# Performance work log

Hardware: AMD Instinct MI355X
Metric: run time of the kernel (lower is better)

Reference implementation:

```python
import jax, jax.numpy as jnp
import numpy as np
from jax import lax

B, C, H, W = 64, 1, 256, 256
N = H * W
K = 16384  # positive_trials
LOG_CLAMP = -100.0  # torch BCELoss clamps log terms at -100


def setup_inputs() -> dict:
    key = jax.random.key(0)
    k1, k2, k3 = jax.random.split(key, 3)
    decision_scores = jax.random.normal(k1, (B, N, 2), dtype=jnp.float32)
    s_map = jax.random.uniform(k2, (B, C, H, W), dtype=jnp.float32)
    # gumbel noise g = -log(-log(U)), matching F.gumbel_softmax sampling
    u = jax.random.uniform(k3, (B, N, 2), dtype=jnp.float32, minval=1e-10, maxval=1.0)
    gumbel_noise = -jnp.log(-jnp.log(u))
    return {"decision_scores": decision_scores, "s_map": s_map, "gumbel_noise": gumbel_noise}


def reference(decision_scores, s_map, gumbel_noise):
    # Tokenizer: b c h w -> b (h w) c
    tokens = jnp.transpose(s_map.reshape(B, C, H * W), (0, 2, 1))  # [B, N, 1]
    # soft gumbel-softmax (tau=1, hard=False), keep prob of class 0
    soft = jax.nn.softmax(decision_scores + gumbel_noise, axis=-1)[:, :, 0:1]  # [B, N, 1]
    # top-K salient token indices per sample (descending sort -> top_k)
    _, idx = lax.top_k(tokens[:, :, 0], K)  # [B, K]
    trials = jnp.zeros((B, N), dtype=tokens.dtype)
    trials = trials.at[jnp.arange(B)[:, None], idx].set(1.0)[:, :, None]  # [B, N, 1]
    # BCE with reduction='sum', log clamped at -100 like torch
    log_p = jnp.clip(jnp.log(soft), LOG_CLAMP, None)
    log_1mp = jnp.clip(jnp.log(1.0 - soft), LOG_CLAMP, None)
    loss = -jnp.sum(trials * log_p + (1.0 - trials) * log_1mp)
    return loss
```

## Files before the change

kernel.cpp:

```cpp
#include <hip/hip_runtime.h>
#include <cstdint>

#define BATCH 64
#define NPIX 65536
#define TOPK 16384
#define NB 256
#define SEGS 32
#define WLO 186
#define WHI 198
#define NWBIN (WHI - WLO + 1)
#define CAPB 192
#define NSLOT (SEGS * CAPB)
#define FCAP 1024
#define WHSTRIDE 16

__device__ __forceinline__ float block_reduce(float acc) {
    __shared__ float w[4];
    __syncthreads();
    #pragma unroll
    for (int off = 32; off > 0; off >>= 1) acc += __shfl_down(acc, off, 64);
    if ((threadIdx.x & 63) == 0) w[threadIdx.x >> 6] = acc;
    __syncthreads();
    return w[0] + w[1] + w[2] + w[3];
}

__device__ __forceinline__ float block_reduce1k(float acc) {
    __shared__ float w[16];
    __syncthreads();
    #pragma unroll
    for (int off = 32; off > 0; off >>= 1) acc += __shfl_down(acc, off, 64);
    if ((threadIdx.x & 63) == 0) w[threadIdx.x >> 6] = acc;
    __syncthreads();
    float s = 0.f;
    #pragma unroll
    for (int i = 0; i < 16; ++i) s += w[i];
    return s;
}

__device__ __forceinline__ void bce_from_d(float d, float& lp, float& llp) {
    float t = __logf(1.f + __expf(-fabsf(d)));
    lp  = fmaxf(fminf(d, 0.f) - t, -100.f);
    llp = fmaxf(-fmaxf(d, 0.f) - t, -100.f);
}

__device__ __forceinline__ int vkey(float v) {
    return (int)fminf(v * 256.0f, 255.0f);
}

__device__ __forceinline__ void stage_candidate(
    bool inwin, float v, uint32_t pix, float diff, int lane,
    uint32_t* ccount, uint32_t* bvb, uint32_t* bvi, uint32_t* bvd)
{
    unsigned long long m = __ballot(inwin);
    if (m == 0ull) return;
    uint32_t cnt = (uint32_t)__popcll(m);
    int leader = (int)__builtin_ctzll(m);
    uint32_t base = 0u;
    if (lane == leader) base = atomicAdd(ccount, cnt);
    base = (uint32_t)__shfl((int)base, leader, 64);
    if (inwin) {
        uint32_t p = base + (uint32_t)__popcll(m & ((1ull << lane) - 1ull));
        if (p < CAPB) {
            bvb[p] = __float_as_uint(v);
            bvi[p] = pix;
            bvd[p] = __float_as_uint(diff);
        }
    }
}

__global__ __launch_bounds__(256, 8) void k1_pass(
    const float4* __restrict__ sc, const float4* __restrict__ gn,
    const float2* __restrict__ tokp,
    float* __restrict__ pk1, float* __restrict__ psel, float* __restrict__ phi,
    uint32_t* __restrict__ gcc,
    uint32_t* __restrict__ cvb, uint32_t* __restrict__ cvi,
    uint32_t* __restrict__ cvd, uint32_t* __restrict__ whist,
    float* __restrict__ out)
{
    __shared__ uint32_t bvb[CAPB], bvi[CAPB], bvd[CAPB];
    __shared__ uint32_t sh_wh[NWBIN];
    __shared__ uint32_t ccount;
    const int tid  = threadIdx.x;
    const int lane = tid & 63;
    if (tid < CAPB) { bvb[tid] = 0u; bvi[tid] = 0u; bvd[tid] = 0u; }
    if (tid < NWBIN) sh_wh[tid] = 0u;
    if (tid == 0) { ccount = 0u; if (blockIdx.x == 0) out[0] = 0.f; }
    __syncthreads();

    const int b   = blockIdx.x >> 5;
    const int seg = blockIdx.x & (SEGS - 1);
    const int pairbase = b * (NPIX / 2) + seg * 1024;

    float4 S[4], G[4];
    float2 T[4];
    #pragma unroll
    for (int it = 0; it < 4; ++it) {
        int j = pairbase + it * 256 + tid;
        S[it] = sc[j];
        G[it] = gn[j];
        T[it] = tokp[j];
    }

    float acc = 0.f, asel = 0.f, chi = 0.f;
    #pragma unroll
    for (int it = 0; it < 4; ++it) {
        int px0 = (seg * 1024 + it * 256 + tid) * 2;
        {
            float d = (S[it].x + G[it].x) - (S[it].y + G[it].y);
            float lp, llp; bce_from_d(d, lp, llp);
            acc += llp;
            float diff = lp - llp;
            int k = vkey(T[it].x);
            bool hi = (k > WHI);
            asel += hi ? diff : 0.f;
            chi  += hi ? 1.f : 0.f;
            stage_candidate(!hi && (k >= WLO), T[it].x, (uint32_t)px0, diff,
                            lane, &ccount, bvb, bvi, bvd);
        }
        {
            float d = (S[it].z + G[it].z) - (S[it].w + G[it].w);
            float lp, llp; bce_from_d(d, lp, llp);
            acc += llp;
            float diff = lp - llp;
            int k = vkey(T[it].y);
            bool hi = (k > WHI);
            asel += hi ? diff : 0.f;
            chi  += hi ? 1.f : 0.f;
            stage_candidate(!hi && (k >= WLO), T[it].y, (uint32_t)(px0 + 1), diff,
                            lane, &ccount, bvb, bvi, bvd);
        }
    }
    __syncthreads();
    const uint32_t cc = ccount;
    {
        uint32_t nsl = cc < CAPB ? cc : CAPB;
        if (tid < nsl) {
            int k = vkey(__uint_as_float(bvb[tid]));
            atomicAdd(&sh_wh[k - WLO], 1u);
        }
    }
    const size_t cbase = (size_t)blockIdx.x * CAPB;
    if (tid < CAPB) {
        cvb[cbase + tid] = bvb[tid];
        cvi[cbase + tid] = bvi[tid];
        cvd[cbase + tid] = bvd[tid];
    }
    if (tid == 0) gcc[blockIdx.x] = cc;

    float t1 = block_reduce(acc);
    float t2 = block_reduce(asel);
    float t3 = block_reduce(chi);
    if (tid == 0) {
        pk1[blockIdx.x]  = t1;
        psel[blockIdx.x] = t2;
        phi[blockIdx.x]  = t3;
    }
    if (tid < NWBIN) whist[(size_t)blockIdx.x * WHSTRIDE + tid] = sh_wh[tid];
}

__global__ __launch_bounds__(1024) void k4_finalize(
    const uint32_t* __restrict__ cvb, const uint32_t* __restrict__ cvi,
    const uint32_t* __restrict__ cvd, const uint32_t* __restrict__ gcc,
    const float* __restrict__ pk1, const float* __restrict__ psel,
    const float* __restrict__ phi, const uint32_t* __restrict__ whist,
    const float4* __restrict__ tok4,
    const float2* __restrict__ sc2, const float2* __restrict__ gn2,
    float* __restrict__ out)
{
    __shared__ uint32_t fvb[FCAP], fvi[FCAP];
    __shared__ float    fdf[FCAP];
    __shared__ uint32_t fh[NB];
    __shared__ uint32_t wc[NWBIN];
    __shared__ uint32_t fcnt;
    __shared__ int      sh_sb, sh_ovf;
    __shared__ uint32_t sh_rem;

    const int b = blockIdx.x, tid = threadIdx.x;
    if (tid == 0) { fcnt = 0u; sh_sb = -1; sh_ovf = 0; sh_rem = 1u; }
    __syncthreads();

    const size_t base = (size_t)b * NSLOT;

    if (tid < SEGS && gcc[b * SEGS + tid] > CAPB) sh_ovf = 1;
    if (tid < NWBIN) {
        uint32_t u = 0;
        #pragma unroll
        for (int s = 0; s < SEGS; ++s)
            u += whist[(size_t)(b * SEGS + s) * WHSTRIDE + tid];
        wc[tid] = u;
    }
    float chl = (tid < SEGS) ? phi[b * SEGS + tid] : 0.f;
    float chf = block_reduce1k(chl);
    if (tid == 0) {
        uint32_t cnt_hi = (uint32_t)(chf + 0.5f);
        if (cnt_hi >= TOPK) sh_ovf = 1;
        else {
            uint32_t cum = cnt_hi;
            int found = -1; uint32_t rem = 1u;
            for (int jj = WHI; jj >= WLO; --jj) {
                uint32_t nc = cum + wc[jj - WLO];
                if (nc >= TOPK) { found = jj; rem = TOPK - cum; break; }
                cum = nc;
            }
            if (found < 0) sh_ovf = 1;
            else { sh_sb = found; sh_rem = rem; }
        }
    }
    __syncthreads();

    bool fast = (sh_ovf == 0);
    const int sb = sh_sb;
    float fac = (tid < SEGS) ? pk1[b * SEGS + tid] : 0.f;

    if (fast) {
        if (tid < SEGS) fac += psel[b * SEGS + tid];
        #pragma unroll
        for (int it = 0; it < NSLOT / 1024; ++it) {
            int t = it * 1024 + tid;
            uint32_t vb = cvb[base + t];
            uint32_t vd = cvd[base + t];
            int k = vkey(__uint_as_float(vb));
            if (k > sb) fac += __uint_as_float(vd);
            else if (k == sb) {
                uint32_t p = atomicAdd(&fcnt, 1u);
                if (p < FCAP) {
                    fvb[p] = vb;
                    fvi[p] = cvi[base + t] & (NPIX - 1);
                    fdf[p] = __uint_as_float(vd);
                }
            }
        }
        __syncthreads();
        if (fcnt > FCAP) fast = false;
        if (fast) {
            const uint32_t cnt = fcnt, rem = sh_rem;
            for (uint32_t j = tid; j < cnt; j += 1024) {
                const uint32_t mb = fvb[j], mi = fvi[j];
                uint32_t rank = 0;
                for (uint32_t i = 0; i < cnt; ++i) {
                    uint32_t ob = fvb[i];
                    rank += (ob > mb) || (ob == mb && fvi[i] < mi);
                }
                if (rank < rem) fac += fdf[j];
            }
        }
    }

    if (!fast) {
        fac = (tid < SEGS) ? pk1[b * SEGS + tid] : 0.f;
        for (int i = tid; i < NB; i += 1024) fh[i] = 0u;
        if (tid == 0) fcnt = 0u;
        __syncthreads();
        const float4* tbase = tok4 + (size_t)b * (NPIX / 4);
        for (int it = 0; it < NPIX / 4 / 1024; ++it) {
            float4 v = tbase[it * 1024 + tid];
            atomicAdd(&fh[vkey(v.x)], 1u);
            atomicAdd(&fh[vkey(v.y)], 1u);
            atomicAdd(&fh[vkey(v.z)], 1u);
            atomicAdd(&fh[vkey(v.w)], 1u);
        }
        __syncthreads();
        if (tid == 0) {
            uint32_t cum = 0; int bin = NB - 1;
            for (; bin > 0; --bin) {
                if (cum + fh[bin] >= TOPK) break;
                cum += fh[bin];
            }
            sh_sb = bin; sh_rem = TOPK - cum;
        }
        __syncthreads();
        const int sb2 = sh_sb; const uint32_t rem2 = sh_rem;
        for (int it = 0; it < NPIX / 4 / 1024; ++it) {
            int j = it * 1024 + tid;
            float4 v = tbase[j];
            int px = j * 4;
            float fv[4] = {v.x, v.y, v.z, v.w};
            #pragma unroll
            for (int q = 0; q < 4; ++q) {
                int k = vkey(fv[q]);
                if (k > sb2) {
                    size_t idx = (size_t)b * NPIX + (px + q);
                    float2 Sv = sc2[idx]; float2 Gv = gn2[idx];
                    float d = (Sv.x + Gv.x) - (Sv.y + Gv.y);
                    float lp, llp; bce_from_d(d, lp, llp);
                    fac += lp - llp;
                } else if (k == sb2) {
                    uint32_t p = atomicAdd(&fcnt, 1u);
                    if (p < FCAP) { fvb[p] = __float_as_uint(fv[q]); fvi[p] = (uint32_t)(px + q); }
                }
            }
        }
        __syncthreads();
        const uint32_t cnt2 = min(fcnt, (uint32_t)FCAP);
        for (uint32_t j = tid; j < cnt2; j += 1024) {
            const uint32_t mb = fvb[j], mi = fvi[j];
            uint32_t rank = 0;
            for (uint32_t i = 0; i < cnt2; ++i) {
                uint32_t ob = fvb[i];
                rank += (ob > mb) || (ob == mb && fvi[i] < mi);
            }
            if (rank < rem2) {
                size_t idx = (size_t)b * NPIX + (mi & (NPIX - 1));
                float2 Sv = sc2[idx]; float2 Gv = gn2[idx];
                float d = (Sv.x + Gv.x) - (Sv.y + Gv.y);
                float lp, llp; bce_from_d(d, lp, llp);
                fac += lp - llp;
            }
        }
    }

    float tot = block_reduce1k(fac);
    if (tid == 0) atomicAdd(out, -tot);
}

extern "C" void kernel_launch(void* const* d_in, const int* in_sizes, int n_in,
                              void* d_out, int out_size, void* d_ws, size_t ws_size,
                              hipStream_t stream) {
    const float* scores = (const float*)d_in[0];
    const float* smap   = (const float*)d_in[1];
    const float* gumbel = (const float*)d_in[2];
    float* out = (float*)d_out;

    char* ws = (char*)d_ws;
    float*    pk1   = (float*)ws;    ws += (size_t)BATCH * SEGS * 4;
    float*    psel  = (float*)ws;    ws += (size_t)BATCH * SEGS * 4;
    float*    phi   = (float*)ws;    ws += (size_t)BATCH * SEGS * 4;
    uint32_t* gcc   = (uint32_t*)ws; ws += (size_t)BATCH * SEGS * 4;
    uint32_t* cvb   = (uint32_t*)ws; ws += (size_t)BATCH * NSLOT * 4;
    uint32_t* cvi   = (uint32_t*)ws; ws += (size_t)BATCH * NSLOT * 4;
    uint32_t* cvd   = (uint32_t*)ws; ws += (size_t)BATCH * NSLOT * 4;
    uint32_t* whist = (uint32_t*)ws; ws += (size_t)BATCH * SEGS * WHSTRIDE * 4;

    k1_pass<<<BATCH * SEGS, 256, 0, stream>>>(
        (const float4*)scores, (const float4*)gumbel, (const float2*)smap,
        pk1, psel, phi, gcc, cvb, cvi, cvd, whist, out);

    k4_finalize<<<BATCH, 1024, 0, stream>>>(
        cvb, cvi, cvd, gcc, pk1, psel, phi, whist,
        (const float4*)smap, (const float2*)scores, (const float2*)gumbel, out);
}
```

Baseline: 118.7 us.

## Bucket-sort candidates by key bin in pass one and sum per-bin diffs

The first kernel now counting-sorts each block's staged candidates by window bin in shared memory and records per-bin sums of the BCE difference. The finalize kernel then adds whole bins above the split bin from those sums and reads only the candidates in the split bin, instead of scanning all 6144 slots per sample. This cuts global reads and branching in the single-block-per-sample finalize step. In exchange the first kernel gains extra barriers, shared atomics and a serial prefix scan.

New measurement: 117.3 us. About the same (-1.2%).

```diff
diff --git a/kernel.cpp b/kernel.cpp
--- a/kernel.cpp
+++ b/kernel.cpp
@@ -75,15 +75,18 @@
     uint32_t* __restrict__ gcc,
     uint32_t* __restrict__ cvb, uint32_t* __restrict__ cvi,
     uint32_t* __restrict__ cvd, uint32_t* __restrict__ whist,
+    float* __restrict__ wdsumg,
     float* __restrict__ out)
 {
     __shared__ uint32_t bvb[CAPB], bvi[CAPB], bvd[CAPB];
-    __shared__ uint32_t sh_wh[NWBIN];
+    __shared__ uint32_t qvb[CAPB], qvi[CAPB], qvd[CAPB];
+    __shared__ uint32_t sh_wh[NWBIN], sh_pref[NWBIN], sh_cur[NWBIN];
+    __shared__ float    sh_wds[NWBIN];
     __shared__ uint32_t ccount;
     const int tid  = threadIdx.x;
     const int lane = tid & 63;
-    if (tid < CAPB) { bvb[tid] = 0u; bvi[tid] = 0u; bvd[tid] = 0u; }
-    if (tid < NWBIN) sh_wh[tid] = 0u;
+    if (tid < CAPB) { qvb[tid] = 0u; qvi[tid] = 0u; qvd[tid] = 0u; }
+    if (tid < NWBIN) { sh_wh[tid] = 0u; sh_cur[tid] = 0u; sh_wds[tid] = 0.f; }
     if (tid == 0) { ccount = 0u; if (blockIdx.x == 0) out[0] = 0.f; }
     __syncthreads();
 
@@ -131,19 +134,34 @@
         }
     }
     __syncthreads();
-    const uint32_t cc = ccount;
-    {
-        uint32_t nsl = cc < CAPB ? cc : CAPB;
-        if (tid < nsl) {
-            int k = vkey(__uint_as_float(bvb[tid]));
-            atomicAdd(&sh_wh[k - WLO], 1u);
-        }
-    }
+    const uint32_t cc  = ccount;
+    const uint32_t nsl = cc < CAPB ? cc : CAPB;
+    if (tid < nsl) {
+        int k = vkey(__uint_as_float(bvb[tid]));
+        atomicAdd(&sh_wh[k - WLO], 1u);
+    }
+    __syncthreads();
+    if (tid == 0) {
+        uint32_t run = 0;
+        #pragma unroll
+        for (int i = 0; i < NWBIN; ++i) { sh_pref[i] = run; run += sh_wh[i]; }
+    }
+    __syncthreads();
+    if (tid < nsl) {
+        uint32_t vb = bvb[tid];
+        int bin = vkey(__uint_as_float(vb)) - WLO;
+        uint32_t pos = sh_pref[bin] + atomicAdd(&sh_cur[bin], 1u);
+        qvb[pos] = vb;
+        qvi[pos] = bvi[tid];
+        qvd[pos] = bvd[tid];
+        atomicAdd(&sh_wds[bin], __uint_as_float(bvd[tid]));
+    }
+    __syncthreads();
     const size_t cbase = (size_t)blockIdx.x * CAPB;
     if (tid < CAPB) {
-        cvb[cbase + tid] = bvb[tid];
-        cvi[cbase + tid] = bvi[tid];
-        cvd[cbase + tid] = bvd[tid];
+        cvb[cbase + tid] = qvb[tid];
+        cvi[cbase + tid] = qvi[tid];
+        cvd[cbase + tid] = qvd[tid];
     }
     if (tid == 0) gcc[blockIdx.x] = cc;
 
@@ -155,7 +173,10 @@
         psel[blockIdx.x] = t2;
         phi[blockIdx.x]  = t3;
     }
-    if (tid < NWBIN) whist[(size_t)blockIdx.x * WHSTRIDE + tid] = sh_wh[tid];
+    if (tid < NWBIN) {
+        whist[(size_t)blockIdx.x * WHSTRIDE + tid]  = sh_wh[tid];
+        wdsumg[(size_t)blockIdx.x * WHSTRIDE + tid] = sh_wds[tid];
+    }
 }
 
 __global__ __launch_bounds__(1024) void k4_finalize(
@@ -163,6 +184,7 @@
     const uint32_t* __restrict__ cvd, const uint32_t* __restrict__ gcc,
     const float* __restrict__ pk1, const float* __restrict__ psel,
     const float* __restrict__ phi, const uint32_t* __restrict__ whist,
+    const float* __restrict__ wdsumg,
     const float4* __restrict__ tok4,
     const float2* __restrict__ sc2, const float2* __restrict__ gn2,
     float* __restrict__ out)
@@ -171,6 +193,7 @@
     __shared__ float    fdf[FCAP];
     __shared__ uint32_t fh[NB];
     __shared__ uint32_t wc[NWBIN];
+    __shared__ uint32_t segstart[SEGS], segcnt[SEGS];
     __shared__ uint32_t fcnt;
     __shared__ int      sh_sb, sh_ovf;
     __shared__ uint32_t sh_rem;
@@ -178,8 +201,6 @@
     const int b = blockIdx.x, tid = threadIdx.x;
     if (tid == 0) { fcnt = 0u; sh_sb = -1; sh_ovf = 0; sh_rem = 1u; }
     __syncthreads();
-
-    const size_t base = (size_t)b * NSLOT;
 
     if (tid < SEGS && gcc[b * SEGS + tid] > CAPB) sh_ovf = 1;
     if (tid < NWBIN) {
@@ -209,24 +230,35 @@
     __syncthreads();
 
     bool fast = (sh_ovf == 0);
-    const int sb = sh_sb;
+    const int sb  = sh_sb;
+    const int sbi = sb - WLO;
     float fac = (tid < SEGS) ? pk1[b * SEGS + tid] : 0.f;
 
     if (fast) {
         if (tid < SEGS) fac += psel[b * SEGS + tid];
-        #pragma unroll
-        for (int it = 0; it < NSLOT / 1024; ++it) {
-            int t = it * 1024 + tid;
-            uint32_t vb = cvb[base + t];
-            uint32_t vd = cvd[base + t];
-            int k = vkey(__uint_as_float(vb));
-            if (k > sb) fac += __uint_as_float(vd);
-            else if (k == sb) {
+        if (tid < SEGS * WHSTRIDE) {
+            int s = tid >> 4, bin = tid & 15;
+            if (bin < NWBIN && bin > sbi)
+                fac += wdsumg[(size_t)(b * SEGS + s) * WHSTRIDE + bin];
+        }
+        if (tid < SEGS) {
+            uint32_t st = 0;
+            for (int i = 0; i < sbi; ++i)
+                st += whist[(size_t)(b * SEGS + tid) * WHSTRIDE + i];
+            segstart[tid] = st;
+            segcnt[tid]   = whist[(size_t)(b * SEGS + tid) * WHSTRIDE + sbi];
+        }
+        __syncthreads();
+        {
+            int g = tid >> 5, l32 = tid & 31;
+            uint32_t c = segcnt[g];
+            size_t sbase = (size_t)(b * SEGS + g) * CAPB + segstart[g];
+            for (uint32_t i = l32; i < c; i += 32) {
                 uint32_t p = atomicAdd(&fcnt, 1u);
                 if (p < FCAP) {
-                    fvb[p] = vb;
-                    fvi[p] = cvi[base + t] & (NPIX - 1);
-                    fdf[p] = __uint_as_float(vd);
+                    fvb[p] = cvb[sbase + i];
+                    fvi[p] = cvi[sbase + i] & (NPIX - 1);
+                    fdf[p] = __uint_as_float(cvd[sbase + i]);
                 }
             }
         }
@@ -330,12 +362,13 @@
     uint32_t* cvi   = (uint32_t*)ws; ws += (size_t)BATCH * NSLOT * 4;
     uint32_t* cvd   = (uint32_t*)ws; ws += (size_t)BATCH * NSLOT * 4;
     uint32_t* whist = (uint32_t*)ws; ws += (size_t)BATCH * SEGS * WHSTRIDE * 4;
+    float*    wdsum = (float*)ws;    ws += (size_t)BATCH * SEGS * WHSTRIDE * 4;
 
     k1_pass<<<BATCH * SEGS, 256, 0, stream>>>(
         (const float4*)scores, (const float4*)gumbel, (const float2*)smap,
-        pk1, psel, phi, gcc, cvb, cvi, cvd, whist, out);
+        pk1, psel, phi, gcc, cvb, cvi, cvd, whist, wdsum, out);
 
     k4_finalize<<<BATCH, 1024, 0, stream>>>(
-        cvb, cvi, cvd, gcc, pk1, psel, phi, whist,
+        cvb, cvi, cvd, gcc, pk1, psel, phi, whist, wdsum,
         (const float4*)smap, (const float2*)scores, (const float2*)gumbel, out);
 }
```
